# Performance work log

Hardware: AMD Instinct MI355X
Metric: run time of the kernel (lower is better)

Reference implementation:

```python
import jax, jax.numpy as jnp
import numpy as np

EMB = 512
HEADS = 8
B, T = 8, 1024

def setup_inputs() -> dict:
    key = jax.random.key(0)
    ks = jax.random.split(key, 6)
    e, h = EMB, HEADS
    s = 1.0 / np.sqrt(e)
    x = jax.random.normal(ks[0], (B, T, e), dtype=jnp.float32)
    # Linear(emb, emb*heads, bias=False): stored as (e, e*h) for x @ W
    Wk = jax.random.normal(ks[1], (e, e * h), dtype=jnp.float32) * s
    Wq = jax.random.normal(ks[2], (e, e * h), dtype=jnp.float32) * s
    Wv = jax.random.normal(ks[3], (e, e * h), dtype=jnp.float32) * s
    # unifyheads: Linear(heads*emb, emb) with bias
    Wu = jax.random.normal(ks[4], (e * h, e), dtype=jnp.float32) * (1.0 / np.sqrt(e * h))
    bu = jax.random.normal(ks[5], (e,), dtype=jnp.float32) * 0.01
    return {"x": x, "Wk": Wk, "Wq": Wq, "Wv": Wv, "Wu": Wu, "bu": bu}

def reference(x, Wk, Wq, Wv, Wu, bu):
    b, t, e = x.shape
    h = HEADS
    scale = e ** (-0.25)  # applied to both q and k, as in the torch code
    q = (x @ Wq).reshape(b, t, h, e) * scale  # (b,t,h,e)
    k = (x @ Wk).reshape(b, t, h, e) * scale
    v = (x @ Wv).reshape(b, t, h, e)
    dot = jnp.einsum('bqhe,bkhe->bhqk', q, k)      # (b,h,t,t)
    attn = jax.nn.softmax(dot, axis=-1)
    out = jnp.einsum('bhqk,bkhe->bqhe', attn, v)    # (b,t,h,e)
    out = out.reshape(b, t, h * e)
    return out @ Wu + bu                            # (b,t,e)
```

## Files before the change

### kernel.cpp

```cpp
#include <hip/hip_runtime.h>
#include <hip/hip_bf16.h>
#include <cstdint>

typedef __attribute__((ext_vector_type(8))) short bf16x8;
typedef __attribute__((ext_vector_type(4))) float f32x4;

typedef __attribute__((address_space(1))) const void gv_t;
typedef __attribute__((address_space(3))) void lv_t;

__device__ __forceinline__ unsigned short f2b(float f) {
  __hip_bfloat16 h = __float2bfloat16(f);
  return __builtin_bit_cast(unsigned short, h);
}
__device__ __forceinline__ float b2f(unsigned short u) {
  unsigned int x = (unsigned int)u << 16;
  return __builtin_bit_cast(float, x);
}

__global__ __launch_bounds__(256) void k_cast(const float* __restrict__ src,
                                              unsigned short* __restrict__ dst, int n4) {
  int i = blockIdx.x * 256 + threadIdx.x;
  if (i >= n4) return;
  const float4 v = ((const float4*)src)[i];
  ushort4 o;
  o.x = f2b(v.x); o.y = f2b(v.y); o.z = f2b(v.z); o.w = f2b(v.w);
  ((ushort4*)dst)[i] = o;
}

__global__ void k_transpose_cast(const float* __restrict__ src,
                                 unsigned short* __restrict__ dst, int R, int C) {
  __shared__ float tile[32][33];
  const int tx = threadIdx.x, ty = threadIdx.y;
  const int c0 = blockIdx.x * 32, r0 = blockIdx.y * 32;
#pragma unroll
  for (int i = 0; i < 32; i += 8)
    tile[ty + i][tx] = src[(long)(r0 + ty + i) * C + (c0 + tx)];
  __syncthreads();
#pragma unroll
  for (int i = 0; i < 32; i += 8)
    dst[(long)(c0 + ty + i) * R + (r0 + tx)] = f2b(tile[tx][ty + i]);
}

__global__ void k_transpose_cast3(const float* __restrict__ s0, const float* __restrict__ s1,
                                  const float* __restrict__ s2,
                                  unsigned short* __restrict__ dst, int R, int C) {
  const float* src = (blockIdx.z == 0) ? s0 : ((blockIdx.z == 1) ? s1 : s2);
  unsigned short* d = dst + (size_t)blockIdx.z * R * C;
  __shared__ float tile[32][33];
  const int tx = threadIdx.x, ty = threadIdx.y;
  const int c0 = blockIdx.x * 32, r0 = blockIdx.y * 32;
#pragma unroll
  for (int i = 0; i < 32; i += 8)
    tile[ty + i][tx] = src[(long)(r0 + ty + i) * C + (c0 + tx)];
  __syncthreads();
#pragma unroll
  for (int i = 0; i < 32; i += 8)
    d[(long)(c0 + ty + i) * R + (r0 + tx)] = f2b(tile[tx][ty + i]);
}

__global__ __launch_bounds__(256) void k_rowsum(const unsigned short* __restrict__ E,
                                                float* __restrict__ rs) {
  const long row = blockIdx.x;
  const unsigned short* p = E + row * 1024;
  const int tid = threadIdx.x;
  const ushort4 raw = ((const ushort4*)p)[tid];
  float s = (b2f(raw.x) + b2f(raw.y)) + (b2f(raw.z) + b2f(raw.w));
#pragma unroll
  for (int off = 32; off >= 1; off >>= 1) s += __shfl_xor(s, off, 64);
  __shared__ float red[4];
  if ((tid & 63) == 0) red[tid >> 6] = s;
  __syncthreads();
  if (tid == 0) rs[row] = (red[0] + red[1]) + (red[2] + red[3]);
}

enum { EPI_QK = 0, EPI_VT = 1, EPI_S = 2, EPI_PV = 3, EPI_OUT = 4 };


#define BAR256() do { asm volatile("" ::: "memory"); __builtin_amdgcn_s_barrier(); asm volatile("" ::: "memory"); } while (0)
#define WAITVM(n) do { asm volatile("s_waitcnt vmcnt(" #n ")" ::: "memory"); __builtin_amdgcn_sched_barrier(0); } while (0)

#define STAGE_A(tt, hw, qq)                                                                     \
  __builtin_amdgcn_global_load_lds(                                                            \
    (gv_t*)(A + (long)(m0 + (hw)*128 + (qq)*64 + rr) * lda + ((tt) << 6) + csw),               \
    (lv_t*)(&L[(((((tt)&1)*2 + (hw))*128 + (qq)*64 + rr))*64 + c0]), 16, 0, 0)

#define STAGE_B(tt, qi)                                                                         \
  __builtin_amdgcn_global_load_lds(                                                            \
    (gv_t*)(Bt + (long)(n0 + (qi)*64 + rr) * ldb + ((tt) << 6) + csw),                         \
    (lv_t*)(&L[32768 + (((((tt)&1)*2 + ((qi)>>1))*128 + ((qi)&1)*64 + rr))*64 + c0]), 16, 0, 0)

#define PHASE(slot, QR, QC) do {                                                                \
    const unsigned short* Abase = &L[((slot)*2 + wr) * 8192];                                   \
    const unsigned short* Bbase = &L[32768 + ((slot)*2 + (wc>>1)) * 8192];                      \
    bf16x8 afr[4][2], bfr[2][2];                                                                \
    _Pragma("unroll")                                                                           \
    for (int fr = 0; fr < 4; ++fr) {                                                            \
      const int rA = (QR)*64 + fr*16 + l15;                                                     \
      _Pragma("unroll")                                                                         \
      for (int kk = 0; kk < 2; ++kk) {                                                          \
        const int cA = (kk*32 + l4*8) ^ ((rA & 7) << 3);                                        \
        afr[fr][kk] = *(const bf16x8*)(Abase + rA*64 + cA);                                     \
      }                                                                                         \
    }                                                                                           \
    _Pragma("unroll")                                                                           \
    for (int fc = 0; fc < 2; ++fc) {                                                            \
      const int rB = (wc&1)*64 + (QC)*32 + fc*16 + l15;                                         \
      _Pragma("unroll")                                                                         \
      for (int kk = 0; kk < 2; ++kk) {                                                          \
        const int cB = (kk*32 + l4*8) ^ ((rB & 7) << 3);                                        \
        bfr[fc][kk] = *(const bf16x8*)(Bbase + rB*64 + cB);                                     \
      }                                                                                         \
    }                                                                                           \
    __builtin_amdgcn_s_setprio(1);                                                              \
    _Pragma("unroll")                                                                           \
    for (int fr = 0; fr < 4; ++fr)                                                              \
      _Pragma("unroll")                                                                         \
      for (int fc = 0; fc < 2; ++fc)                                                            \
        _Pragma("unroll")                                                                       \
        for (int kk = 0; kk < 2; ++kk)                                                          \
          acc[(QR)*4+fr][(QC)*2+fc] = __builtin_amdgcn_mfma_f32_16x16x32_bf16(                  \
              afr[fr][kk], bfr[fc][kk], acc[(QR)*4+fr][(QC)*2+fc], 0, 0, 0);                    \
    __builtin_amdgcn_s_setprio(0);                                                              \
  } while (0)

template <int EPI>
__global__ __launch_bounds__(512)
void k_gemm256(const unsigned short* __restrict__ A, const unsigned short* __restrict__ Bt,
               void* __restrict__ Cv, int K, int lda, int ldb,
               long sA, long sB, float scale, const float* __restrict__ aux) {
  const int z = blockIdx.z;
  A += (long)z * sA;
  Bt += (long)z * sB;
  const int m0 = blockIdx.y * 256;
  const int n0 = blockIdx.x * 256;
  __shared__ __align__(16) unsigned short L[65536];
  const int tid = threadIdx.x;
  const int lane = tid & 63;
  const int wid = tid >> 6;
  const int wr = wid >> 2;
  const int wc = wid & 3;
  const int l15 = lane & 15;
  const int l4 = lane >> 4;
  const int rr = tid >> 3;
  const int c0 = (tid & 7) * 8;
  const int csw = c0 ^ ((rr & 7) << 3);

  f32x4 acc[8][4] = {};
  const int NT = K >> 6;

  STAGE_A(0, 0, 0); STAGE_A(0, 1, 0); STAGE_A(0, 0, 1); STAGE_A(0, 1, 1);
  STAGE_B(0, 0); STAGE_B(0, 1); STAGE_B(0, 2); STAGE_B(0, 3);
  if (NT > 1) {
    STAGE_A(1, 0, 0); STAGE_A(1, 1, 0);
    WAITVM(2);
  } else {
    WAITVM(0);
  }
  __builtin_amdgcn_s_barrier();
  asm volatile("" ::: "memory");

  for (int t = 0; t < NT; ++t) {
    const int slot = t & 1;
    if (t + 1 < NT) { STAGE_A(t + 1, 0, 1); STAGE_A(t + 1, 1, 1); }
    PHASE(slot, 0, 0);
    BAR256();
    if (t + 1 < NT) { STAGE_B(t + 1, 0); STAGE_B(t + 1, 1); }
    PHASE(slot, 0, 1);
    BAR256();
    if (t + 1 < NT) { STAGE_B(t + 1, 2); STAGE_B(t + 1, 3); }
    if (t + 2 < NT) { STAGE_A(t + 2, 0, 0); STAGE_A(t + 2, 1, 0); }
    PHASE(slot, 1, 0);
    BAR256();
    PHASE(slot, 1, 1);
    if (t + 1 < NT) {
      if (t + 2 < NT) WAITVM(2);
      else            WAITVM(0);
      __builtin_amdgcn_s_barrier();
      asm volatile("" ::: "memory");
    }
  }

#pragma unroll
  for (int i = 0; i < 8; ++i) {
#pragma unroll
    for (int j = 0; j < 4; ++j) {
#pragma unroll
      for (int r = 0; r < 4; ++r) {
        const int row = m0 + wr * 128 + i * 16 + l4 * 4 + r;
        const int col = n0 + wc * 64 + j * 16 + l15;
        const float v = acc[i][j][r];
        if (EPI == EPI_QK) {
          unsigned short* o = (unsigned short*)Cv;
          const int sec = col >> 12;
          const int cc = col & 4095;
          const long addr = (long)sec * 33554432 +
              ((long)((row >> 10) * 8 + (cc >> 9)) * 1024 + (row & 1023)) * 512 + (cc & 511);
          o[addr] = f2b(v * scale);
        } else if (EPI == EPI_VT) {
          unsigned short* o = (unsigned short*)Cv;
          const long addr = (long)((col >> 10) * 8 + (row >> 9)) * 524288 +
                            (long)(row & 511) * 1024 + (col & 1023);
          o[addr] = f2b(v);
        }
      }
    }
  }
}

template <int EPI>
__global__ __launch_bounds__(256)
void k_gemm(const unsigned short* __restrict__ A, const unsigned short* __restrict__ Bt,
            void* __restrict__ Cv, int K, int lda, int ldb,
            long sA, long sB, float scale, const float* __restrict__ aux) {
  const int z = blockIdx.z;
  A += (long)z * sA;
  Bt += (long)z * sB;
  const int m0 = blockIdx.y * 128;
  const int n0 = blockIdx.x * 128;
  __shared__ __align__(16) unsigned short As[2][128 * 32];
  __shared__ __align__(16) unsigned short Bs[2][128 * 32];
  const int tid = threadIdx.x;
  const int lane = tid & 63;
  const int wm = ((tid >> 6) >> 1) * 64;
  const int wn = ((tid >> 6) & 1) * 64;
  const int srow = tid >> 2;
  const int scol = (tid & 3) * 8;
  f32x4 acc[4][4] = {};

  const unsigned short* ga = A + (long)(m0 + srow) * lda + scol;
  const unsigned short* gb = Bt + (long)(n0 + srow) * ldb + scol;

#define STAGE(buf, koff) do {                                                                        \
    __builtin_amdgcn_global_load_lds((gv_t*)(ga + (koff)), (lv_t*)(&As[buf][tid * 8]), 16, 0, 0);     \
    __builtin_amdgcn_global_load_lds((gv_t*)(ga + 64L * lda + (koff)), (lv_t*)(&As[buf][tid * 8 + 2048]), 16, 0, 0); \
    __builtin_amdgcn_global_load_lds((gv_t*)(gb + (koff)), (lv_t*)(&Bs[buf][tid * 8]), 16, 0, 0);     \
    __builtin_amdgcn_global_load_lds((gv_t*)(gb + 64L * ldb + (koff)), (lv_t*)(&Bs[buf][tid * 8 + 2048]), 16, 0, 0); \
  } while (0)

  STAGE(0, 0);
  for (int k0 = 0; k0 < K; k0 += 32) {
    const int cur = (k0 >> 5) & 1;
    __syncthreads();
    if (k0 + 32 < K) { STAGE(cur ^ 1, k0 + 32); }
    const unsigned short* ap = &As[cur][(wm + (lane & 15)) * 32 + (lane >> 4) * 8];
    const unsigned short* bp = &Bs[cur][(wn + (lane & 15)) * 32 + (lane >> 4) * 8];
    bf16x8 fa[4], fb[4];
#pragma unroll
    for (int i = 0; i < 4; ++i) fa[i] = *(const bf16x8*)(ap + i * 16 * 32);
#pragma unroll
    for (int i = 0; i < 4; ++i) fb[i] = *(const bf16x8*)(bp + i * 16 * 32);
#pragma unroll
    for (int mi = 0; mi < 4; ++mi)
#pragma unroll
      for (int ni = 0; ni < 4; ++ni)
        acc[mi][ni] = __builtin_amdgcn_mfma_f32_16x16x32_bf16(fa[mi], fb[ni], acc[mi][ni], 0, 0, 0);
  }
#undef STAGE

#pragma unroll
  for (int mi = 0; mi < 4; ++mi) {
#pragma unroll
    for (int ni = 0; ni < 4; ++ni) {
#pragma unroll
      for (int r = 0; r < 4; ++r) {
        const int row = m0 + wm + mi * 16 + ((lane >> 4) * 4 + r);
        const int col = n0 + wn + ni * 16 + (lane & 15);
        const float v = acc[mi][ni][r];
        if (EPI == EPI_S) {
          unsigned short* o = (unsigned short*)Cv;
          o[(long)z * 1048576 + (long)row * 1024 + col] = f2b(__expf(v));
        } else if (EPI == EPI_PV) {
          unsigned short* o = (unsigned short*)Cv;
          const float val = v / aux[(long)z * 1024 + row];
          const long addr = (long)(z >> 3) * 4194304 + (long)row * 4096 + (long)(z & 7) * 512 + col;
          o[addr] = f2b(val);
        } else {
          float* o = (float*)Cv;
          o[(long)row * 512 + col] = v + aux[col];
        }
      }
    }
  }
}

extern "C" void kernel_launch(void* const* d_in, const int* in_sizes, int n_in,
                              void* d_out, int out_size, void* d_ws, size_t ws_size,
                              hipStream_t stream) {
  const float* x  = (const float*)d_in[0];
  const float* Wk = (const float*)d_in[1];
  const float* Wq = (const float*)d_in[2];
  const float* Wv = (const float*)d_in[3];
  const float* Wu = (const float*)d_in[4];
  const float* bu = (const float*)d_in[5];
  float* out = (float*)d_out;
  char* ws = (char*)d_ws;

  const size_t NEED1 = 243302400;
  const size_t NEED2 = 260112384;
  const size_t NEED4 = 293732352;
  if (ws_size < NEED1) return;
  const int CH = (ws_size >= NEED4) ? 4 : ((ws_size >= NEED2) ? 2 : 1);

  unsigned short* wut   = (unsigned short*)(ws + 0);
  unsigned short* wtqkv = (unsigned short*)(ws + 4194304);
  unsigned short* xb    = (unsigned short*)(ws + 16777216);
  unsigned short* qb    = (unsigned short*)(ws + 25165824);
  unsigned short* kb    = qb + 33554432;
  unsigned short* vtb   = qb + 67108864;
  unsigned short* Sbuf  = (unsigned short*)(ws + 226492416);
  float*          rs    = (float*)(Sbuf + (size_t)CH * 8388608);

  const float s4 = 0.21022410381342865f;

  k_cast<<<4096, 256, 0, stream>>>(x, xb, 1048576);
  k_transpose_cast3<<<dim3(128, 16, 3), dim3(32, 8), 0, stream>>>(Wq, Wk, Wv, wtqkv, 512, 4096);
  k_transpose_cast<<<dim3(16, 128), dim3(32, 8), 0, stream>>>(Wu, wut, 4096, 512);

  k_gemm256<EPI_QK><<<dim3(32, 32, 1), 512, 0, stream>>>(xb, wtqkv, qb, 512, 512, 512, 0, 0, s4, nullptr);
  k_gemm256<EPI_VT><<<dim3(32, 16, 1), 512, 0, stream>>>(wtqkv + 4194304, xb, vtb, 512, 512, 512, 0, 0, 1.0f, nullptr);

  for (int b = 0; b < 8; b += CH) {
    const long aoff = (long)b * 4194304;
    k_gemm<EPI_S><<<dim3(8, 8, CH * 8), 256, 0, stream>>>(qb + aoff, kb + aoff, Sbuf,
                                                          512, 512, 512, 524288, 524288, 1.0f, nullptr);
    k_rowsum<<<CH * 8192, 256, 0, stream>>>(Sbuf, rs);
    k_gemm<EPI_PV><<<dim3(4, 8, CH * 8), 256, 0, stream>>>(Sbuf, vtb + aoff, qb + aoff,
                                                           1024, 1024, 1024, 1048576, 524288, 1.0f, rs);
  }

  k_gemm<EPI_OUT><<<dim3(4, 64, 1), 256, 0, stream>>>(qb, wut, out, 4096, 4096, 4096, 0, 0, 1.0f, bu);
}
```

Before: 532.8 us.

## Fuse QK^T, exp, rowsum and PV into a single flash-style attention kernel

Replaces the separate S=QK^T GEMM, rowsum kernel and PV GEMM (which round-tripped the full exp-score matrix through global memory) with one fused attention kernel per (head, 64-query tile). The kernel streams K and V^T in 32-key chunks through LDS, computes exp scores into a small LDS tile, accumulates row sums and the PV product in registers, then normalizes and writes into the q buffer in head-major layout. The output GEMM is rewritten to read that head-major layout directly. It skips max subtraction, as the original did, and the inner loop uses small tiles with several barriers per chunk, which may limit MFMA utilization.

```diff
diff --git a/kernel.cpp b/kernel.cpp
--- a/kernel.cpp
+++ b/kernel.cpp
@@ -58,23 +58,7 @@
     d[(long)(c0 + ty + i) * R + (r0 + tx)] = f2b(tile[tx][ty + i]);
 }
 
-__global__ __launch_bounds__(256) void k_rowsum(const unsigned short* __restrict__ E,
-                                                float* __restrict__ rs) {
-  const long row = blockIdx.x;
-  const unsigned short* p = E + row * 1024;
-  const int tid = threadIdx.x;
-  const ushort4 raw = ((const ushort4*)p)[tid];
-  float s = (b2f(raw.x) + b2f(raw.y)) + (b2f(raw.z) + b2f(raw.w));
-#pragma unroll
-  for (int off = 32; off >= 1; off >>= 1) s += __shfl_xor(s, off, 64);
-  __shared__ float red[4];
-  if ((tid & 63) == 0) red[tid >> 6] = s;
-  __syncthreads();
-  if (tid == 0) rs[row] = (red[0] + red[1]) + (red[2] + red[3]);
-}
-
-enum { EPI_QK = 0, EPI_VT = 1, EPI_S = 2, EPI_PV = 3, EPI_OUT = 4 };
-
+enum { EPI_QK = 0, EPI_VT = 1 };
 
 #define BAR256() do { asm volatile("" ::: "memory"); __builtin_amdgcn_s_barrier(); asm volatile("" ::: "memory"); } while (0)
 #define WAITVM(n) do { asm volatile("s_waitcnt vmcnt(" #n ")" ::: "memory"); __builtin_amdgcn_sched_barrier(0); } while (0)
@@ -126,11 +110,7 @@
 template <int EPI>
 __global__ __launch_bounds__(512)
 void k_gemm256(const unsigned short* __restrict__ A, const unsigned short* __restrict__ Bt,
-               void* __restrict__ Cv, int K, int lda, int ldb,
-               long sA, long sB, float scale, const float* __restrict__ aux) {
-  const int z = blockIdx.z;
-  A += (long)z * sA;
-  Bt += (long)z * sB;
+               void* __restrict__ Cv, int K, int lda, int ldb, float scale) {
   const int m0 = blockIdx.y * 256;
   const int n0 = blockIdx.x * 256;
   __shared__ __align__(16) unsigned short L[65536];
@@ -196,7 +176,7 @@
           const long addr = (long)sec * 33554432 +
               ((long)((row >> 10) * 8 + (cc >> 9)) * 1024 + (row & 1023)) * 512 + (cc & 511);
           o[addr] = f2b(v * scale);
-        } else if (EPI == EPI_VT) {
+        } else {
           unsigned short* o = (unsigned short*)Cv;
           const long addr = (long)((col >> 10) * 8 + (row >> 9)) * 524288 +
                             (long)(row & 511) * 1024 + (col & 1023);
@@ -207,14 +187,131 @@
   }
 }
 
-template <int EPI>
+__global__ __launch_bounds__(512)
+void k_attn(unsigned short* __restrict__ q,
+            const unsigned short* __restrict__ k,
+            const unsigned short* __restrict__ vt)
+{
+  __shared__ __align__(16) unsigned short Qs[64 * 512];
+  __shared__ __align__(16) unsigned short Ks[32 * 512];
+  __shared__ __align__(16) unsigned short Vs[512 * 32];
+  __shared__ __align__(16) unsigned short Es[64 * 32];
+  const int bid = blockIdx.x;
+  const int head = (bid & 7) * 8 + ((bid >> 3) >> 4);
+  const int qt = (bid >> 3) & 15;
+  const int tid = threadIdx.x;
+  const int w = tid >> 6, lane = tid & 63;
+  const int l15 = lane & 15, l4 = lane >> 4;
+  const int qf = w & 3, kf = w >> 2;
+
+  unsigned short* qg = q + (size_t)(head * 1024 + qt * 64) * 512;
+  const unsigned short* kg = k + (size_t)head * 524288;
+  const unsigned short* vg = vt + (size_t)head * 524288;
+
+#pragma unroll
+  for (int i = 0; i < 8; ++i) {
+    const int row = i * 8 + w;
+    __builtin_amdgcn_global_load_lds((gv_t*)(qg + (size_t)row * 512 + 8 * (lane ^ (row & 7))),
+                                     (lv_t*)(&Qs[row * 512 + lane * 8]), 16, 0, 0);
+  }
+#pragma unroll
+  for (int i = 0; i < 4; ++i) {
+    const int row = i * 8 + w;
+    __builtin_amdgcn_global_load_lds((gv_t*)(kg + (size_t)row * 512 + 8 * (lane ^ (row & 7))),
+                                     (lv_t*)(&Ks[row * 512 + lane * 8]), 16, 0, 0);
+  }
+  __syncthreads();
+
+  f32x4 acc[4][4] = {};
+  float partial = 0.f;
+  const int erow = tid >> 3;
+  const int ej = tid & 7;
+  const int eidx = 32 * erow + 8 * ((ej >> 1) ^ (erow & 3)) + (ej & 1) * 4;
+  const int qrow = qf * 16 + l15;
+  const int krow = kf * 16 + l15;
+
+  for (int c = 0; c < 32; ++c) {
+#pragma unroll
+    for (int i = 0; i < 4; ++i) {
+      const int r0 = i * 128 + w * 16;
+      const int e = r0 + (lane >> 2);
+      __builtin_amdgcn_global_load_lds(
+          (gv_t*)(vg + (size_t)e * 1024 + c * 32 + 8 * ((lane & 3) ^ (e & 3))),
+          (lv_t*)(&Vs[r0 * 32 + lane * 8]), 16, 0, 0);
+    }
+    f32x4 sacc = {0.f, 0.f, 0.f, 0.f};
+#pragma unroll
+    for (int ks = 0; ks < 16; ++ks) {
+      bf16x8 aq = *(const bf16x8*)(&Qs[qrow * 512 + 8 * ((ks * 4 + l4) ^ (qrow & 7))]);
+      bf16x8 bk = *(const bf16x8*)(&Ks[krow * 512 + 8 * ((ks * 4 + l4) ^ (krow & 7))]);
+      sacc = __builtin_amdgcn_mfma_f32_16x16x32_bf16(aq, bk, sacc, 0, 0, 0);
+    }
+#pragma unroll
+    for (int r = 0; r < 4; ++r) {
+      const int qq = qf * 16 + l4 * 4 + r;
+      const int kk2 = kf * 16 + l15;
+      Es[32 * qq + (kk2 & 7) + 8 * ((kk2 >> 3) ^ (qq & 3))] = f2b(__expf(sacc[r]));
+    }
+    __syncthreads();
+    if (c + 1 < 32) {
+#pragma unroll
+      for (int i = 0; i < 4; ++i) {
+        const int row = i * 8 + w;
+        __builtin_amdgcn_global_load_lds(
+            (gv_t*)(kg + (size_t)((c + 1) * 32 + row) * 512 + 8 * (lane ^ (row & 7))),
+            (lv_t*)(&Ks[row * 512 + lane * 8]), 16, 0, 0);
+      }
+    }
+    {
+      const ushort4 ev = *(const ushort4*)(&Es[eidx]);
+      partial += (b2f(ev.x) + b2f(ev.y)) + (b2f(ev.z) + b2f(ev.w));
+    }
+    bf16x8 bv[4];
+#pragma unroll
+    for (int cf = 0; cf < 4; ++cf) {
+      const int e = w * 64 + cf * 16 + l15;
+      bv[cf] = *(const bf16x8*)(&Vs[e * 32 + 8 * (l4 ^ (e & 3))]);
+    }
+#pragma unroll
+    for (int qf2 = 0; qf2 < 4; ++qf2) {
+      const int qq = qf2 * 16 + l15;
+      bf16x8 ae = *(const bf16x8*)(&Es[32 * qq + 8 * (l4 ^ (qq & 3))]);
+#pragma unroll
+      for (int cf = 0; cf < 4; ++cf)
+        acc[qf2][cf] = __builtin_amdgcn_mfma_f32_16x16x32_bf16(ae, bv[cf], acc[qf2][cf], 0, 0, 0);
+    }
+    __syncthreads();
+  }
+
+  float* fs = (float*)Ks;
+  fs[tid] = partial;
+  __syncthreads();
+  if (tid < 64) {
+    float s = 0.f;
+#pragma unroll
+    for (int j = 0; j < 8; ++j) s += fs[tid * 8 + j];
+    fs[512 + tid] = 1.0f / s;
+  }
+  __syncthreads();
+
+#pragma unroll
+  for (int qf2 = 0; qf2 < 4; ++qf2) {
+#pragma unroll
+    for (int r = 0; r < 4; ++r) {
+      const int qq = qf2 * 16 + l4 * 4 + r;
+      const float iv = fs[512 + qq];
+#pragma unroll
+      for (int cf = 0; cf < 4; ++cf) {
+        const int e = w * 64 + cf * 16 + l15;
+        qg[(size_t)qq * 512 + e] = f2b(acc[qf2][cf][r] * iv);
+      }
+    }
+  }
+}
+
 __global__ __launch_bounds__(256)
-void k_gemm(const unsigned short* __restrict__ A, const unsigned short* __restrict__ Bt,
-            void* __restrict__ Cv, int K, int lda, int ldb,
-            long sA, long sB, float scale, const float* __restrict__ aux) {
-  const int z = blockIdx.z;
-  A += (long)z * sA;
-  Bt += (long)z * sB;
+void k_gemm_out(const unsigned short* __restrict__ A, const unsigned short* __restrict__ Bt,
+                float* __restrict__ C, const float* __restrict__ bias) {
   const int m0 = blockIdx.y * 128;
   const int n0 = blockIdx.x * 128;
   __shared__ __align__(16) unsigned short As[2][128 * 32];
@@ -227,21 +324,24 @@
   const int scol = (tid & 3) * 8;
   f32x4 acc[4][4] = {};
 
-  const unsigned short* ga = A + (long)(m0 + srow) * lda + scol;
-  const unsigned short* gb = Bt + (long)(n0 + srow) * ldb + scol;
-
-#define STAGE(buf, koff) do {                                                                        \
-    __builtin_amdgcn_global_load_lds((gv_t*)(ga + (koff)), (lv_t*)(&As[buf][tid * 8]), 16, 0, 0);     \
-    __builtin_amdgcn_global_load_lds((gv_t*)(ga + 64L * lda + (koff)), (lv_t*)(&As[buf][tid * 8 + 2048]), 16, 0, 0); \
-    __builtin_amdgcn_global_load_lds((gv_t*)(gb + (koff)), (lv_t*)(&Bs[buf][tid * 8]), 16, 0, 0);     \
-    __builtin_amdgcn_global_load_lds((gv_t*)(gb + 64L * ldb + (koff)), (lv_t*)(&Bs[buf][tid * 8 + 2048]), 16, 0, 0); \
+  const int row1 = m0 + srow, row2 = row1 + 64;
+  const size_t hb1 = (size_t)(row1 >> 10) * 8 * 524288 + (size_t)(row1 & 1023) * 512;
+  const size_t hb2 = (size_t)(row2 >> 10) * 8 * 524288 + (size_t)(row2 & 1023) * 512;
+  const unsigned short* gb = Bt + (size_t)(n0 + srow) * 4096 + scol;
+
+#define STAGEO(buf, k0) do {                                                                          \
+    const size_t koffA = (size_t)((k0) >> 9) * 524288 + ((k0) & 511) + scol;                          \
+    __builtin_amdgcn_global_load_lds((gv_t*)(A + hb1 + koffA), (lv_t*)(&As[buf][tid * 8]), 16, 0, 0);  \
+    __builtin_amdgcn_global_load_lds((gv_t*)(A + hb2 + koffA), (lv_t*)(&As[buf][tid * 8 + 2048]), 16, 0, 0); \
+    __builtin_amdgcn_global_load_lds((gv_t*)(gb + (k0)), (lv_t*)(&Bs[buf][tid * 8]), 16, 0, 0);        \
+    __builtin_amdgcn_global_load_lds((gv_t*)(gb + 64L * 4096 + (k0)), (lv_t*)(&Bs[buf][tid * 8 + 2048]), 16, 0, 0); \
   } while (0)
 
-  STAGE(0, 0);
-  for (int k0 = 0; k0 < K; k0 += 32) {
+  STAGEO(0, 0);
+  for (int k0 = 0; k0 < 4096; k0 += 32) {
     const int cur = (k0 >> 5) & 1;
     __syncthreads();
-    if (k0 + 32 < K) { STAGE(cur ^ 1, k0 + 32); }
+    if (k0 + 32 < 4096) { STAGEO(cur ^ 1, k0 + 32); }
     const unsigned short* ap = &As[cur][(wm + (lane & 15)) * 32 + (lane >> 4) * 8];
     const unsigned short* bp = &Bs[cur][(wn + (lane & 15)) * 32 + (lane >> 4) * 8];
     bf16x8 fa[4], fb[4];
@@ -255,7 +355,7 @@
       for (int ni = 0; ni < 4; ++ni)
         acc[mi][ni] = __builtin_amdgcn_mfma_f32_16x16x32_bf16(fa[mi], fb[ni], acc[mi][ni], 0, 0, 0);
   }
-#undef STAGE
+#undef STAGEO
 
 #pragma unroll
   for (int mi = 0; mi < 4; ++mi) {
@@ -265,19 +365,7 @@
       for (int r = 0; r < 4; ++r) {
         const int row = m0 + wm + mi * 16 + ((lane >> 4) * 4 + r);
         const int col = n0 + wn + ni * 16 + (lane & 15);
-        const float v = acc[mi][ni][r];
-        if (EPI == EPI_S) {
-          unsigned short* o = (unsigned short*)Cv;
-          o[(long)z * 1048576 + (long)row * 1024 + col] = f2b(__expf(v));
-        } else if (EPI == EPI_PV) {
-          unsigned short* o = (unsigned short*)Cv;
-          const float val = v / aux[(long)z * 1024 + row];
-          const long addr = (long)(z >> 3) * 4194304 + (long)row * 4096 + (long)(z & 7) * 512 + col;
-          o[addr] = f2b(val);
-        } else {
-          float* o = (float*)Cv;
-          o[(long)row * 512 + col] = v + aux[col];
-        }
+        C[(long)row * 512 + col] = acc[mi][ni][r] + bias[col];
       }
     }
   }
@@ -295,11 +383,8 @@
   float* out = (float*)d_out;
   char* ws = (char*)d_ws;
 
-  const size_t NEED1 = 243302400;
-  const size_t NEED2 = 260112384;
-  const size_t NEED4 = 293732352;
-  if (ws_size < NEED1) return;
-  const int CH = (ws_size >= NEED4) ? 4 : ((ws_size >= NEED2) ? 2 : 1);
+  const size_t NEED = 226492416;
+  if (ws_size < NEED) return;
 
   unsigned short* wut   = (unsigned short*)(ws + 0);
   unsigned short* wtqkv = (unsigned short*)(ws + 4194304);
@@ -307,8 +392,6 @@
   unsigned short* qb    = (unsigned short*)(ws + 25165824);
   unsigned short* kb    = qb + 33554432;
   unsigned short* vtb   = qb + 67108864;
-  unsigned short* Sbuf  = (unsigned short*)(ws + 226492416);
-  float*          rs    = (float*)(Sbuf + (size_t)CH * 8388608);
 
   const float s4 = 0.21022410381342865f;
 
@@ -316,17 +399,10 @@
   k_transpose_cast3<<<dim3(128, 16, 3), dim3(32, 8), 0, stream>>>(Wq, Wk, Wv, wtqkv, 512, 4096);
   k_transpose_cast<<<dim3(16, 128), dim3(32, 8), 0, stream>>>(Wu, wut, 4096, 512);
 
-  k_gemm256<EPI_QK><<<dim3(32, 32, 1), 512, 0, stream>>>(xb, wtqkv, qb, 512, 512, 512, 0, 0, s4, nullptr);
-  k_gemm256<EPI_VT><<<dim3(32, 16, 1), 512, 0, stream>>>(wtqkv + 4194304, xb, vtb, 512, 512, 512, 0, 0, 1.0f, nullptr);
-
-  for (int b = 0; b < 8; b += CH) {
-    const long aoff = (long)b * 4194304;
-    k_gemm<EPI_S><<<dim3(8, 8, CH * 8), 256, 0, stream>>>(qb + aoff, kb + aoff, Sbuf,
-                                                          512, 512, 512, 524288, 524288, 1.0f, nullptr);
-    k_rowsum<<<CH * 8192, 256, 0, stream>>>(Sbuf, rs);
-    k_gemm<EPI_PV><<<dim3(4, 8, CH * 8), 256, 0, stream>>>(Sbuf, vtb + aoff, qb + aoff,
-                                                           1024, 1024, 1024, 1048576, 524288, 1.0f, rs);
-  }
-
-  k_gemm<EPI_OUT><<<dim3(4, 64, 1), 256, 0, stream>>>(qb, wut, out, 4096, 4096, 4096, 0, 0, 1.0f, bu);
-}
+  k_gemm256<EPI_QK><<<dim3(32, 32, 1), 512, 0, stream>>>(xb, wtqkv, qb, 512, 512, 512, s4);
+  k_gemm256<EPI_VT><<<dim3(32, 16, 1), 512, 0, stream>>>(wtqkv + 4194304, xb, vtb, 512, 512, 512, 1.0f);
+
+  k_attn<<<1024, 512, 0, stream>>>(qb, kb, vtb);
+
+  k_gemm_out<<<dim3(4, 64, 1), 256, 0, stream>>>(qb, wut, out, bu);
+}
```

After: 503.1 us. -5.6%, faster.
